# Kernel tuning notes

Hardware: AMD Instinct MI355X
Metric: run time of the kernel (lower is better)

## Reference

```python
import jax, jax.numpy as jnp
import numpy as np

E = 8          # num_experts
K = 2          # top_k
ALPHA = 0.01   # aux_loss_coef


def setup_inputs() -> dict:
    key = jax.random.key(0)
    k1, k2, k3, k4 = jax.random.split(key, 4)
    x = jax.random.normal(k1, (4, 4096, 768), jnp.float32)
    gate_w = jax.random.normal(k2, (E, 768), jnp.float32) * 0.02   # Router gate [E, H]
    w1 = jax.random.normal(k3, (E, 3072, 768), jnp.float32) * 0.02  # per-expert [I, H]
    w2 = jax.random.normal(k4, (E, 768, 3072), jnp.float32) * 0.02  # per-expert [H, I]
    return {"x": x, "gate_w": gate_w, "w1": w1, "w2": w2}


def reference(x, gate_w, w1, w2):
    B, S, H = x.shape
    N = B * S
    x_flat = x.reshape(N, H)

    # ---- Router: top-K gating ----
    gate_logits = x_flat @ gate_w.T                      # [N, E]
    gate_probs = jax.nn.softmax(gate_logits, axis=-1)    # [N, E]
    top_weights, top_indices = jax.lax.top_k(gate_probs, K)  # [N, K] each
    top_weights = top_weights / top_weights.sum(-1, keepdims=True)

    # ---- Load balancing aux loss ----
    counts = jnp.zeros(E, gate_probs.dtype).at[top_indices.reshape(-1)].add(1.0)
    f = counts / (N * K)
    p = gate_probs.mean(axis=0)
    aux_loss = ALPHA * E * jnp.sum(f * p)

    # ---- Dispatch + per-expert FFN + weighted combine ----
    # combine[n, e] = sum_k top_weights[n, k] * [top_indices[n, k] == e]
    combine = jnp.zeros((N, E), x_flat.dtype).at[
        jnp.arange(N)[:, None], top_indices
    ].add(top_weights)                                   # [N, E]

    y = jnp.zeros_like(x_flat)
    for e in range(E):  # fixed small loop over experts
        h = jax.nn.gelu(x_flat @ w1[e].T, approximate=True)  # [N, I] (GELU-tanh)
        y = y + combine[:, e:e + 1] * (h @ w2[e].T)          # [N, H]

    return y.reshape(B, S, H), aux_loss
```

## Files before the change

### kernel.cpp

```cpp
#include <hip/hip_runtime.h>
#include <hip/hip_bf16.h>

#define N_TOK 16384
#define H_DIM 768
#define I_DIM 3072
#define NEXP 8
#define RBLK 1024

typedef short bf16x8 __attribute__((ext_vector_type(8)));
typedef float f32x4 __attribute__((ext_vector_type(4)));

__device__ __forceinline__ unsigned short f2bf(float f) {
    unsigned int u = __float_as_uint(f);
    u += 0x7fffu + ((u >> 16) & 1u);
    return (unsigned short)(u >> 16);
}

__device__ __forceinline__ float gelu_tanh(float v) {
    float u = 0.7978845608028654f * (v + 0.044715f * v * v * v);
    float t = __expf(2.0f * fminf(u, 15.0f));
    return 0.5f * v * (1.0f + (t - 1.0f) / (t + 1.0f));
}

__device__ __forceinline__ void gll16(const void* g, void* l) {
    __builtin_amdgcn_global_load_lds(
        (const __attribute__((address_space(1))) unsigned int*)g,
        (__attribute__((address_space(3))) unsigned int*)l, 16, 0, 0);
}

__global__ __launch_bounds__(256) void moe_router(
    const float* __restrict__ x, const float* __restrict__ gw,
    unsigned short* __restrict__ xbf,
    int* __restrict__ topidx, float* __restrict__ topw,
    float* __restrict__ partials)
{
    __shared__ float gws[NEXP * H_DIM];
    __shared__ float red[64];
    const int tid = threadIdx.x;
    for (int i = tid * 4; i < NEXP * H_DIM; i += 1024)
        *(float4*)(gws + i) = *(const float4*)(gw + i);
    __syncthreads();

    const int lane = tid & 63;
    const int wid = tid >> 6;
    const int tbase = blockIdx.x * 16 + wid * 4;

    float lcnt[8], lps[8];
#pragma unroll
    for (int e = 0; e < 8; ++e) { lcnt[e] = 0.f; lps[e] = 0.f; }

#pragma unroll
    for (int k = 0; k < 4; ++k) {
        const int t = tbase + k;
        float acc[8] = {0.f, 0.f, 0.f, 0.f, 0.f, 0.f, 0.f, 0.f};
#pragma unroll
        for (int j = 0; j < 3; ++j) {
            const int col = j * 256 + lane * 4;
            float4 xv = *(const float4*)(x + (size_t)t * H_DIM + col);
            ushort4 o;
            o.x = f2bf(xv.x); o.y = f2bf(xv.y); o.z = f2bf(xv.z); o.w = f2bf(xv.w);
            *(ushort4*)(xbf + (size_t)t * H_DIM + col) = o;
#pragma unroll
            for (int e = 0; e < 8; ++e) {
                float4 g = *(const float4*)(gws + e * H_DIM + col);
                acc[e] += xv.x * g.x + xv.y * g.y + xv.z * g.z + xv.w * g.w;
            }
        }
#pragma unroll
        for (int off = 32; off >= 1; off >>= 1)
#pragma unroll
            for (int e = 0; e < 8; ++e) acc[e] += __shfl_xor(acc[e], off, 64);

        int e0 = 0;
#pragma unroll
        for (int e = 1; e < 8; ++e) if (acc[e] > acc[e0]) e0 = e;
        int e1 = (e0 == 0) ? 1 : 0;
#pragma unroll
        for (int e = 0; e < 8; ++e) if (e != e0 && acc[e] > acc[e1]) e1 = e;

        float mx = acc[0];
#pragma unroll
        for (int e = 1; e < 8; ++e) mx = fmaxf(mx, acc[e]);
        float p[8]; float s = 0.f;
#pragma unroll
        for (int e = 0; e < 8; ++e) { p[e] = expf(acc[e] - mx); s += p[e]; }
        float inv = 1.0f / s;
#pragma unroll
        for (int e = 0; e < 8; ++e) p[e] *= inv;

        float wsum = p[e0] + p[e1];
        if (lane == 0) {
            topidx[2 * t] = e0; topidx[2 * t + 1] = e1;
            topw[2 * t] = p[e0] / wsum; topw[2 * t + 1] = p[e1] / wsum;
            lcnt[e0] += 1.f; lcnt[e1] += 1.f;
#pragma unroll
            for (int e = 0; e < 8; ++e) lps[e] += p[e];
        }
    }

    if (lane == 0) {
#pragma unroll
        for (int e = 0; e < 8; ++e) {
            red[wid * 16 + e] = lcnt[e];
            red[wid * 16 + 8 + e] = lps[e];
        }
    }
    __syncthreads();
    if (tid < 16)
        partials[blockIdx.x * 16 + tid] =
            red[tid] + red[16 + tid] + red[32 + tid] + red[48 + tid];
}

__global__ __launch_bounds__(256) void moe_finalize(
    const float* __restrict__ partials, int* __restrict__ offs,
    float* __restrict__ aux_out)
{
    __shared__ float sdata[256];
    __shared__ float tot[16];
    const int tid = threadIdx.x;
    const int c = tid & 15;
    const int rg = tid >> 4;
    float s = 0.f;
    for (int r = rg; r < RBLK; r += 16)
        s += partials[r * 16 + c];
    sdata[tid] = s;
    __syncthreads();
    if (tid < 16) {
        float t = 0.f;
#pragma unroll
        for (int k = 0; k < 16; ++k) t += sdata[k * 16 + tid];
        tot[tid] = t;
    }
    __syncthreads();
    if (tid == 0) {
        float aux = 0.f; int run = 0;
        for (int e = 0; e < 8; ++e) {
            float cnt = tot[e];
            aux += (cnt / (float)(N_TOK * 2)) * (tot[8 + e] / (float)N_TOK);
            offs[e] = run;
            run += (int)(cnt + 0.5f);
        }
        offs[8] = run;
        *aux_out = 0.01f * 8.0f * aux;
    }
}

__global__ __launch_bounds__(256) void moe_rank(
    const int* __restrict__ topidx, const float* __restrict__ topw,
    const float* __restrict__ partials, const int* __restrict__ offs,
    int* __restrict__ perm, float* __restrict__ pw)
{
    const int b = blockIdx.x;
    const int tid = threadIdx.x;
    __shared__ float sred[256];
    __shared__ int pfx[8];
    float s = 0.f;
    const int e = tid & 7;
    for (int r = (tid >> 3); r < b; r += 32)
        s += partials[r * 16 + e];
    sred[tid] = s;
    __syncthreads();
    if (tid < 8) {
        float t = 0.f;
        for (int k = tid; k < 256; k += 8) t += sred[k];
        pfx[tid] = offs[tid] + (int)(t + 0.5f);
    }
    __syncthreads();
    if (tid < 32) {
        const int t = b * 16 + (tid >> 1);
        const int slot = tid & 1;
        const int myexp = topidx[2 * t + slot];
        int rank = 0;
#pragma unroll
        for (int ee = 0; ee < 8; ++ee) {
            unsigned long long m = __ballot(myexp == ee);
            if (myexp == ee)
                rank = pfx[ee] + __popcll(m & ((1ull << tid) - 1ull));
        }
        perm[rank] = t;
        pw[rank] = topw[2 * t + slot];
    }
}

__global__ __launch_bounds__(256) void moe_cvt(const float* __restrict__ in,
                                               unsigned short* __restrict__ out, int n)
{
    int idx = (blockIdx.x * 256 + threadIdx.x) * 4;
    const int stride = gridDim.x * 1024;
    for (; idx < n; idx += stride) {
        float4 v = *(const float4*)(in + idx);
        ushort4 o;
        o.x = f2bf(v.x); o.y = f2bf(v.y); o.z = f2bf(v.z); o.w = f2bf(v.w);
        *(ushort4*)(out + idx) = o;
    }
}


__global__ __launch_bounds__(256) void moe_gemm1(
    const unsigned short* __restrict__ xbf,
    const unsigned short* __restrict__ w1bf,
    const int* __restrict__ perm, const int* __restrict__ offs,
    unsigned short* __restrict__ hbuf, int e0)
{
    const int e = e0 + blockIdx.z;
    const int off = offs[e];
    const int n_e = offs[e + 1] - off;
    const int rt = blockIdx.y;
    if (rt * 128 >= n_e) return;
    const int ct = blockIdx.x;
    const int coff = off - offs[e0];

    __shared__ __align__(16) unsigned short As[128 * 64];
    __shared__ __align__(16) unsigned short Bs[128 * 64];

    const int tid = threadIdx.x;
    const int lane = tid & 63;
    const int wid = tid >> 6;
    const int wr = wid >> 1, wc = wid & 1;
    const int trow = tid >> 3;
    const int tcol = (((tid & 7) ^ (trow & 7))) * 8;

    const unsigned short* aptr[4];
    const unsigned short* bptr[4];
#pragma unroll
    for (int i = 0; i < 4; ++i) {
        int lr = rt * 128 + i * 32 + trow;
        if (lr >= n_e) lr = n_e - 1;
        const int token = perm[off + lr];
        aptr[i] = xbf + (size_t)token * H_DIM + tcol;
        const int n = ct * 128 + i * 32 + trow;
        bptr[i] = w1bf + ((size_t)e * I_DIM + n) * H_DIM + tcol;
    }
    unsigned short* As_dst = As + tid * 8;
    unsigned short* Bs_dst = Bs + tid * 8;

    const int rA = (wr * 64 + (lane & 15)) * 64;
    const int rB = (wc * 64 + (lane & 15)) * 64;
    const int cs0 = (((lane >> 4)    ) ^ (lane & 7)) * 8;
    const int cs1 = (((lane >> 4) + 4) ^ (lane & 7)) * 8;

    f32x4 acc[4][4] = {};

    for (int kk = 0; kk < H_DIM; kk += 64) {
#pragma unroll
        for (int i = 0; i < 4; ++i) gll16(aptr[i] + kk, As_dst + i * 2048);
#pragma unroll
        for (int i = 0; i < 4; ++i) gll16(bptr[i] + kk, Bs_dst + i * 2048);
        __syncthreads();
#pragma unroll
        for (int ksub = 0; ksub < 2; ++ksub) {
            const int cs = ksub ? cs1 : cs0;
            bf16x8 a[4], b[4];
#pragma unroll
            for (int i = 0; i < 4; ++i) a[i] = *(const bf16x8*)(As + rA + i * 1024 + cs);
#pragma unroll
            for (int j = 0; j < 4; ++j) b[j] = *(const bf16x8*)(Bs + rB + j * 1024 + cs);
#pragma unroll
            for (int i = 0; i < 4; ++i)
#pragma unroll
                for (int j = 0; j < 4; ++j)
                    acc[i][j] = __builtin_amdgcn_mfma_f32_16x16x32_bf16(a[i], b[j], acc[i][j], 0, 0, 0);
        }
        __syncthreads();
    }

    const int rbase = rt * 128 + wr * 64 + (lane >> 4) * 4;
    const int cbase = ct * 128 + wc * 64 + (lane & 15);
#pragma unroll
    for (int i = 0; i < 4; ++i) {
#pragma unroll
        for (int r = 0; r < 4; ++r) {
            const int lr = rbase + i * 16 + r;
            if (lr < n_e) {
                unsigned short* dst = hbuf + (size_t)(coff + lr) * I_DIM + cbase;
#pragma unroll
                for (int j = 0; j < 4; ++j)
                    dst[j * 16] = f2bf(gelu_tanh(acc[i][j][r]));
            }
        }
    }
}

__global__ __launch_bounds__(256) void moe_gemm2(
    const unsigned short* __restrict__ hbuf,
    const unsigned short* __restrict__ w2bf,
    const int* __restrict__ perm, const float* __restrict__ pw,
    const int* __restrict__ offs, float* __restrict__ y, int e0)
{
    const int e = e0 + blockIdx.z;
    const int off = offs[e];
    const int n_e = offs[e + 1] - off;
    const int rt = blockIdx.y;
    if (rt * 128 >= n_e) return;
    const int ct = blockIdx.x;
    const int coff = off - offs[e0];

    __shared__ __align__(16) unsigned short As[128 * 64];
    __shared__ __align__(16) unsigned short Bs[128 * 64];

    const int tid = threadIdx.x;
    const int lane = tid & 63;
    const int wid = tid >> 6;
    const int wr = wid >> 1, wc = wid & 1;
    const int trow = tid >> 3;
    const int tcol = (((tid & 7) ^ (trow & 7))) * 8;

    const unsigned short* aptr[4];
    const unsigned short* bptr[4];
#pragma unroll
    for (int i = 0; i < 4; ++i) {
        int lr = rt * 128 + i * 32 + trow;
        if (lr >= n_e) lr = n_e - 1;
        aptr[i] = hbuf + (size_t)(coff + lr) * I_DIM + tcol;
        const int n = ct * 128 + i * 32 + trow;
        bptr[i] = w2bf + ((size_t)e * H_DIM + n) * I_DIM + tcol;
    }
    unsigned short* As_dst = As + tid * 8;
    unsigned short* Bs_dst = Bs + tid * 8;

    const int rA = (wr * 64 + (lane & 15)) * 64;
    const int rB = (wc * 64 + (lane & 15)) * 64;
    const int cs0 = (((lane >> 4)    ) ^ (lane & 7)) * 8;
    const int cs1 = (((lane >> 4) + 4) ^ (lane & 7)) * 8;

    f32x4 acc[4][4] = {};

    for (int kk = 0; kk < I_DIM; kk += 64) {
#pragma unroll
        for (int i = 0; i < 4; ++i) gll16(aptr[i] + kk, As_dst + i * 2048);
#pragma unroll
        for (int i = 0; i < 4; ++i) gll16(bptr[i] + kk, Bs_dst + i * 2048);
        __syncthreads();
#pragma unroll
        for (int ksub = 0; ksub < 2; ++ksub) {
            const int cs = ksub ? cs1 : cs0;
            bf16x8 a[4], b[4];
#pragma unroll
            for (int i = 0; i < 4; ++i) a[i] = *(const bf16x8*)(As + rA + i * 1024 + cs);
#pragma unroll
            for (int j = 0; j < 4; ++j) b[j] = *(const bf16x8*)(Bs + rB + j * 1024 + cs);
#pragma unroll
            for (int i = 0; i < 4; ++i)
#pragma unroll
                for (int j = 0; j < 4; ++j)
                    acc[i][j] = __builtin_amdgcn_mfma_f32_16x16x32_bf16(a[i], b[j], acc[i][j], 0, 0, 0);
        }
        __syncthreads();
    }

    const int rbase = rt * 128 + wr * 64 + (lane >> 4) * 4;
    const int cbase = ct * 128 + wc * 64 + (lane & 15);
#pragma unroll
    for (int i = 0; i < 4; ++i) {
#pragma unroll
        for (int r = 0; r < 4; ++r) {
            const int lr = rbase + i * 16 + r;
            if (lr < n_e) {
                const int token = perm[off + lr];
                const float w = pw[off + lr];
                float* dst = y + (size_t)token * H_DIM + cbase;
#pragma unroll
                for (int j = 0; j < 4; ++j)
                    atomicAdd(dst + j * 16, w * acc[i][j][r]);
            }
        }
    }
}

extern "C" void kernel_launch(void* const* d_in, const int* in_sizes, int n_in,
                              void* d_out, int out_size, void* d_ws, size_t ws_size,
                              hipStream_t stream) {
    const float* x  = (const float*)d_in[0];
    const float* gw = (const float*)d_in[1];
    const float* w1 = (const float*)d_in[2];
    const float* w2 = (const float*)d_in[3];
    float* y = (float*)d_out;

    char* base = (char*)d_ws;
    size_t o = 0;
    unsigned short* xbf  = (unsigned short*)(base + o); o += (size_t)N_TOK * H_DIM * 2;
    unsigned short* w1bf = (unsigned short*)(base + o); o += (size_t)NEXP * I_DIM * H_DIM * 2;
    unsigned short* w2bf = (unsigned short*)(base + o); o += (size_t)NEXP * H_DIM * I_DIM * 2;
    int*   topidx = (int*)(base + o);   o += (size_t)N_TOK * 2 * 4;
    float* topw   = (float*)(base + o); o += (size_t)N_TOK * 2 * 4;
    int*   perm   = (int*)(base + o);   o += (size_t)N_TOK * 2 * 4;
    float* pw     = (float*)(base + o); o += (size_t)N_TOK * 2 * 4;
    float* partials = (float*)(base + o); o += (size_t)RBLK * 16 * 4;
    int*   offs     = (int*)(base + o);   o += 64;
    unsigned short* hbuf = (unsigned short*)(base + o);
    size_t remain = (ws_size > o) ? (ws_size - o) : 0;

    long cap_rows = (long)(remain / (size_t)(I_DIM * 2));
    int nch;
    if (cap_rows >= 32768)      nch = 1;
    else if (cap_rows >= 18022) nch = 2;
    else if (cap_rows >= 9011)  nch = 4;
    else                        nch = 8;
    const int G = NEXP / nch;

    hipMemsetAsync(d_out, 0, (size_t)out_size * 4, stream);

    moe_router<<<RBLK, 256, 0, stream>>>(x, gw, xbf, topidx, topw, partials);

    moe_cvt<<<2048, 256, 0, stream>>>(w1, w1bf, NEXP * I_DIM * H_DIM);
    moe_cvt<<<2048, 256, 0, stream>>>(w2, w2bf, NEXP * H_DIM * I_DIM);

    moe_finalize<<<1, 256, 0, stream>>>(partials, offs, y + (size_t)N_TOK * H_DIM);
    moe_rank<<<RBLK, 256, 0, stream>>>(topidx, topw, partials, offs, perm, pw);

    for (int c = 0; c < nch; ++c) {
        const int e0 = c * G;
        moe_gemm1<<<dim3(24, 128, G), 256, 0, stream>>>(
            xbf, w1bf, perm, offs, hbuf, e0);
        moe_gemm2<<<dim3(6, 128, G), 256, 0, stream>>>(
            hbuf, w2bf, perm, pw, offs, y, e0);
    }
}
```

Baseline: 700.2 us.

## Pipeline expert GEMMs with 4-stage LDS ring and fuse small setup kernels

Both expert GEMMs now use a 4-deep shared-memory ring with K=32 per stage, issuing loads three stages ahead. Waits use explicit vmcnt counters, a single barrier per step and setprio around the MFMA block, so global loads overlap with matrix math instead of a load, sync, compute, sync loop. The finalize kernel is folded into moe_rank, with each block recomputing the totals and block 0 writing offsets and aux loss, and the two weight conversions are merged into one launch. LDS use grows to 64KB per block, which may lower occupancy, and every rank block now reads all partials.

Measured after the change: 678.6 us. 1.03x faster.

```diff
diff --git a/kernel.cpp b/kernel.cpp
--- a/kernel.cpp
+++ b/kernel.cpp
@@ -111,59 +111,45 @@
             red[tid] + red[16 + tid] + red[32 + tid] + red[48 + tid];
 }
 
-__global__ __launch_bounds__(256) void moe_finalize(
-    const float* __restrict__ partials, int* __restrict__ offs,
-    float* __restrict__ aux_out)
-{
-    __shared__ float sdata[256];
-    __shared__ float tot[16];
-    const int tid = threadIdx.x;
-    const int c = tid & 15;
-    const int rg = tid >> 4;
-    float s = 0.f;
-    for (int r = rg; r < RBLK; r += 16)
-        s += partials[r * 16 + c];
-    sdata[tid] = s;
-    __syncthreads();
-    if (tid < 16) {
-        float t = 0.f;
-#pragma unroll
-        for (int k = 0; k < 16; ++k) t += sdata[k * 16 + tid];
-        tot[tid] = t;
-    }
-    __syncthreads();
-    if (tid == 0) {
-        float aux = 0.f; int run = 0;
-        for (int e = 0; e < 8; ++e) {
-            float cnt = tot[e];
-            aux += (cnt / (float)(N_TOK * 2)) * (tot[8 + e] / (float)N_TOK);
-            offs[e] = run;
-            run += (int)(cnt + 0.5f);
-        }
-        offs[8] = run;
-        *aux_out = 0.01f * 8.0f * aux;
-    }
-}
-
 __global__ __launch_bounds__(256) void moe_rank(
     const int* __restrict__ topidx, const float* __restrict__ topw,
-    const float* __restrict__ partials, const int* __restrict__ offs,
-    int* __restrict__ perm, float* __restrict__ pw)
+    const float* __restrict__ partials, int* __restrict__ offs,
+    float* __restrict__ aux_out, int* __restrict__ perm, float* __restrict__ pw)
 {
     const int b = blockIdx.x;
     const int tid = threadIdx.x;
-    __shared__ float sred[256];
+    __shared__ float stot[256], spre[256];
+    __shared__ float tot[16];
     __shared__ int pfx[8];
-    float s = 0.f;
-    const int e = tid & 7;
-    for (int r = (tid >> 3); r < b; r += 32)
-        s += partials[r * 16 + e];
-    sred[tid] = s;
+
+    const int c = tid & 15;
+    float vtot = 0.f, vpre = 0.f;
+    for (int r = tid >> 4; r < RBLK; r += 16) {
+        float v = partials[r * 16 + c];
+        vtot += v;
+        if (r < b) vpre += v;
+    }
+    stot[tid] = vtot; spre[tid] = vpre;
     __syncthreads();
-    if (tid < 8) {
-        float t = 0.f;
-        for (int k = tid; k < 256; k += 8) t += sred[k];
-        pfx[tid] = offs[tid] + (int)(t + 0.5f);
+    if (tid < 16) {
+        float t = 0.f, q = 0.f;
+#pragma unroll
+        for (int k = 0; k < 16; ++k) { t += stot[k * 16 + tid]; q += spre[k * 16 + tid]; }
+        tot[tid] = t;
+        if (tid < 8) spre[tid] = q;
+    }
+    __syncthreads();
+    if (tid == 0) {
+        int run = 0;
+        float aux = 0.f;
+#pragma unroll
+        for (int e = 0; e < 8; ++e) {
+            pfx[e] = run + (int)(spre[e] + 0.5f);
+            aux += (tot[e] / (float)(N_TOK * 2)) * (tot[8 + e] / (float)N_TOK);
+            if (b == 0) offs[e] = run;
+            run += (int)(tot[e] + 0.5f);
+        }
+        if (b == 0) { offs[8] = run; *aux_out = 0.01f * 8.0f * aux; }
     }
     __syncthreads();
     if (tid < 32) {
@@ -182,19 +168,69 @@
     }
 }
 
-__global__ __launch_bounds__(256) void moe_cvt(const float* __restrict__ in,
-                                               unsigned short* __restrict__ out, int n)
+__global__ __launch_bounds__(256) void moe_cvt2(
+    const float* __restrict__ a, unsigned short* __restrict__ oa,
+    const float* __restrict__ bsrc, unsigned short* __restrict__ ob, int n)
 {
     int idx = (blockIdx.x * 256 + threadIdx.x) * 4;
     const int stride = gridDim.x * 1024;
-    for (; idx < n; idx += stride) {
-        float4 v = *(const float4*)(in + idx);
+    for (; idx < 2 * n; idx += stride) {
+        const float* in = (idx < n) ? a : bsrc;
+        unsigned short* out = (idx < n) ? oa : ob;
+        const int i = (idx < n) ? idx : idx - n;
+        float4 v = *(const float4*)(in + i);
         ushort4 o;
         o.x = f2bf(v.x); o.y = f2bf(v.y); o.z = f2bf(v.z); o.w = f2bf(v.w);
-        *(ushort4*)(out + idx) = o;
-    }
-}
-
+        *(ushort4*)(out + i) = o;
+    }
+}
+
+
+#define GEMM_STAGE(t)                                                             \
+    { const int s_ = (t) & 3;                                                     \
+      gll16(asrc0 + (t) * 32, As + s_ * 4096 +        tid * 8);                   \
+      gll16(asrc1 + (t) * 32, As + s_ * 4096 + 2048 + tid * 8);                   \
+      gll16(bsrc0 + (t) * 32, Bs + s_ * 4096 +        tid * 8);                   \
+      gll16(bsrc1 + (t) * 32, Bs + s_ * 4096 + 2048 + tid * 8); }
+
+#define GEMM_LOADFRAG(t)                                                          \
+      const unsigned short* Ab_ = As + ((t) & 3) * 4096 + rowbase + pA * 8;       \
+      const unsigned short* Bb_ = Bs + ((t) & 3) * 4096 + rowbase + pB * 8;       \
+      bf16x8 a_[4], b_[4];                                                        \
+      _Pragma("unroll")                                                           \
+      for (int i_ = 0; i_ < 4; ++i_) a_[i_] = *(const bf16x8*)(Ab_ + i_ * 1024);  \
+      _Pragma("unroll")                                                           \
+      for (int j_ = 0; j_ < 4; ++j_) b_[j_] = *(const bf16x8*)(Bb_ + j_ * 1024);
+
+#define GEMM_MFMA()                                                               \
+      __builtin_amdgcn_s_setprio(1);                                              \
+      _Pragma("unroll")                                                           \
+      for (int i_ = 0; i_ < 4; ++i_)                                              \
+      _Pragma("unroll")                                                           \
+      for (int j_ = 0; j_ < 4; ++j_)                                              \
+          acc[i_][j_] = __builtin_amdgcn_mfma_f32_16x16x32_bf16(                  \
+              a_[i_], b_[j_], acc[i_][j_], 0, 0, 0);                              \
+      __builtin_amdgcn_s_setprio(0);
+
+#define GEMM_SYNC(N_IMM)                                                          \
+    asm volatile("s_waitcnt vmcnt(" #N_IMM ")" ::: "memory");                     \
+    __builtin_amdgcn_s_barrier();                                                 \
+    __builtin_amdgcn_sched_barrier(0);
+
+#define GEMM_PIPELINE(NT)                                                         \
+    GEMM_STAGE(0); GEMM_STAGE(1); GEMM_STAGE(2);                                  \
+    GEMM_SYNC(8);                                                                 \
+    for (int t = 0; t < (NT) - 3; ++t) {                                          \
+        GEMM_LOADFRAG(t);                                                         \
+        GEMM_STAGE(t + 3);                                                        \
+        GEMM_MFMA();                                                              \
+        GEMM_SYNC(8);                                                             \
+    }                                                                             \
+    { GEMM_LOADFRAG((NT) - 3); GEMM_MFMA(); }                                     \
+    GEMM_SYNC(4);                                                                 \
+    { GEMM_LOADFRAG((NT) - 2); GEMM_MFMA(); }                                     \
+    GEMM_SYNC(0);                                                                 \
+    { GEMM_LOADFRAG((NT) - 1); GEMM_MFMA(); }
 
 __global__ __launch_bounds__(256) void moe_gemm1(
     const unsigned short* __restrict__ xbf,
@@ -210,59 +246,37 @@
     const int ct = blockIdx.x;
     const int coff = off - offs[e0];
 
-    __shared__ __align__(16) unsigned short As[128 * 64];
-    __shared__ __align__(16) unsigned short Bs[128 * 64];
+    __shared__ __align__(16) unsigned short As[4 * 4096];
+    __shared__ __align__(16) unsigned short Bs[4 * 4096];
 
     const int tid = threadIdx.x;
     const int lane = tid & 63;
     const int wid = tid >> 6;
     const int wr = wid >> 1, wc = wid & 1;
-    const int trow = tid >> 3;
-    const int tcol = (((tid & 7) ^ (trow & 7))) * 8;
-
-    const unsigned short* aptr[4];
-    const unsigned short* bptr[4];
-#pragma unroll
-    for (int i = 0; i < 4; ++i) {
-        int lr = rt * 128 + i * 32 + trow;
-        if (lr >= n_e) lr = n_e - 1;
-        const int token = perm[off + lr];
-        aptr[i] = xbf + (size_t)token * H_DIM + tcol;
-        const int n = ct * 128 + i * 32 + trow;
-        bptr[i] = w1bf + ((size_t)e * I_DIM + n) * H_DIM + tcol;
-    }
-    unsigned short* As_dst = As + tid * 8;
-    unsigned short* Bs_dst = Bs + tid * 8;
-
-    const int rA = (wr * 64 + (lane & 15)) * 64;
-    const int rB = (wc * 64 + (lane & 15)) * 64;
-    const int cs0 = (((lane >> 4)    ) ^ (lane & 7)) * 8;
-    const int cs1 = (((lane >> 4) + 4) ^ (lane & 7)) * 8;
+
+    const int m = tid >> 3;
+    const int csw = (tid & 7) ^ (m & 7);
+    const int hi = csw >> 2, kc = csw & 3;
+
+    const unsigned short* asrc0; const unsigned short* asrc1;
+    const unsigned short* bsrc0; const unsigned short* bsrc1;
+    {
+        int g0 = hi * 64 + m, g1 = hi * 64 + 32 + m;
+        int lr0 = rt * 128 + g0; if (lr0 >= n_e) lr0 = n_e - 1;
+        int lr1 = rt * 128 + g1; if (lr1 >= n_e) lr1 = n_e - 1;
+        asrc0 = xbf + (size_t)perm[off + lr0] * H_DIM + kc * 8;
+        asrc1 = xbf + (size_t)perm[off + lr1] * H_DIM + kc * 8;
+        bsrc0 = w1bf + ((size_t)e * I_DIM + ct * 128 + g0) * H_DIM + kc * 8;
+        bsrc1 = w1bf + ((size_t)e * I_DIM + ct * 128 + g1) * H_DIM + kc * 8;
+    }
+
+    const int pA = ((wr << 2) | (lane >> 4)) ^ (lane & 7);
+    const int pB = ((wc << 2) | (lane >> 4)) ^ (lane & 7);
+    const int rowbase = (lane & 15) * 64;
 
     f32x4 acc[4][4] = {};
 
-    for (int kk = 0; kk < H_DIM; kk += 64) {
-#pragma unroll
-        for (int i = 0; i < 4; ++i) gll16(aptr[i] + kk, As_dst + i * 2048);
-#pragma unroll
-        for (int i = 0; i < 4; ++i) gll16(bptr[i] + kk, Bs_dst + i * 2048);
-        __syncthreads();
-#pragma unroll
-        for (int ksub = 0; ksub < 2; ++ksub) {
-            const int cs = ksub ? cs1 : cs0;
-            bf16x8 a[4], b[4];
-#pragma unroll
-            for (int i = 0; i < 4; ++i) a[i] = *(const bf16x8*)(As + rA + i * 1024 + cs);
-#pragma unroll
-            for (int j = 0; j < 4; ++j) b[j] = *(const bf16x8*)(Bs + rB + j * 1024 + cs);
-#pragma unroll
-            for (int i = 0; i < 4; ++i)
-#pragma unroll
-                for (int j = 0; j < 4; ++j)
-                    acc[i][j] = __builtin_amdgcn_mfma_f32_16x16x32_bf16(a[i], b[j], acc[i][j], 0, 0, 0);
-        }
-        __syncthreads();
-    }
+    GEMM_PIPELINE(H_DIM / 32);
 
     const int rbase = rt * 128 + wr * 64 + (lane >> 4) * 4;
     const int cbase = ct * 128 + wc * 64 + (lane & 15);
@@ -295,58 +309,37 @@
     const int ct = blockIdx.x;
     const int coff = off - offs[e0];
 
-    __shared__ __align__(16) unsigned short As[128 * 64];
-    __shared__ __align__(16) unsigned short Bs[128 * 64];
+    __shared__ __align__(16) unsigned short As[4 * 4096];
+    __shared__ __align__(16) unsigned short Bs[4 * 4096];
 
     const int tid = threadIdx.x;
     const int lane = tid & 63;
     const int wid = tid >> 6;
     const int wr = wid >> 1, wc = wid & 1;
-    const int trow = tid >> 3;
-    const int tcol = (((tid & 7) ^ (trow & 7))) * 8;
-
-    const unsigned short* aptr[4];
-    const unsigned short* bptr[4];
-#pragma unroll
-    for (int i = 0; i < 4; ++i) {
-        int lr = rt * 128 + i * 32 + trow;
-        if (lr >= n_e) lr = n_e - 1;
-        aptr[i] = hbuf + (size_t)(coff + lr) * I_DIM + tcol;
-        const int n = ct * 128 + i * 32 + trow;
-        bptr[i] = w2bf + ((size_t)e * H_DIM + n) * I_DIM + tcol;
-    }
-    unsigned short* As_dst = As + tid * 8;
-    unsigned short* Bs_dst = Bs + tid * 8;
-
-    const int rA = (wr * 64 + (lane & 15)) * 64;
-    const int rB = (wc * 64 + (lane & 15)) * 64;
-    const int cs0 = (((lane >> 4)    ) ^ (lane & 7)) * 8;
-    const int cs1 = (((lane >> 4) + 4) ^ (lane & 7)) * 8;
+
+    const int m = tid >> 3;
+    const int csw = (tid & 7) ^ (m & 7);
+    const int hi = csw >> 2, kc = csw & 3;
+
+    const unsigned short* asrc0; const unsigned short* asrc1;
+    const unsigned short* bsrc0; const unsigned short* bsrc1;
+    {
+        int g0 = hi * 64 + m, g1 = hi * 64 + 32 + m;
+        int lr0 = rt * 128 + g0; if (lr0 >= n_e) lr0 = n_e - 1;
+        int lr1 = rt * 128 + g1; if (lr1 >= n_e) lr1 = n_e - 1;
+        asrc0 = hbuf + (size_t)(coff + lr0) * I_DIM + kc * 8;
+        asrc1 = hbuf + (size_t)(coff + lr1) * I_DIM + kc * 8;
+        bsrc0 = w2bf + ((size_t)e * H_DIM + ct * 128 + g0) * I_DIM + kc * 8;
+        bsrc1 = w2bf + ((size_t)e * H_DIM + ct * 128 + g1) * I_DIM + kc * 8;
+    }
+
+    const int pA = ((wr << 2) | (lane >> 4)) ^ (lane & 7);
+    const int pB = ((wc << 2) | (lane >> 4)) ^ (lane & 7);
+    const int rowbase = (lane & 15) * 64;
 
     f32x4 acc[4][4] = {};
 
-    for (int kk = 0; kk < I_DIM; kk += 64) {
-#pragma unroll
-        for (int i = 0; i < 4; ++i) gll16(aptr[i] + kk, As_dst + i * 2048);
-#pragma unroll
-        for (int i = 0; i < 4; ++i) gll16(bptr[i] + kk, Bs_dst + i * 2048);
-        __syncthreads();
-#pragma unroll
-        for (int ksub = 0; ksub < 2; ++ksub) {
-            const int cs = ksub ? cs1 : cs0;
-            bf16x8 a[4], b[4];
-#pragma unroll
-            for (int i = 0; i < 4; ++i) a[i] = *(const bf16x8*)(As + rA + i * 1024 + cs);
-#pragma unroll
-            for (int j = 0; j < 4; ++j) b[j] = *(const bf16x8*)(Bs + rB + j * 1024 + cs);
-#pragma unroll
-            for (int i = 0; i < 4; ++i)
-#pragma unroll
-                for (int j = 0; j < 4; ++j)
-                    acc[i][j] = __builtin_amdgcn_mfma_f32_16x16x32_bf16(a[i], b[j], acc[i][j], 0, 0, 0);
-        }
-        __syncthreads();
-    }
+    GEMM_PIPELINE(I_DIM / 32);
 
     const int rbase = rt * 128 + wr * 64 + (lane >> 4) * 4;
     const int cbase = ct * 128 + wc * 64 + (lane & 15);
@@ -401,12 +394,9 @@
     hipMemsetAsync(d_out, 0, (size_t)out_size * 4, stream);
 
     moe_router<<<RBLK, 256, 0, stream>>>(x, gw, xbf, topidx, topw, partials);
-
-    moe_cvt<<<2048, 256, 0, stream>>>(w1, w1bf, NEXP * I_DIM * H_DIM);
-    moe_cvt<<<2048, 256, 0, stream>>>(w2, w2bf, NEXP * H_DIM * I_DIM);
-
-    moe_finalize<<<1, 256, 0, stream>>>(partials, offs, y + (size_t)N_TOK * H_DIM);
-    moe_rank<<<RBLK, 256, 0, stream>>>(topidx, topw, partials, offs, perm, pw);
+    moe_cvt2<<<4096, 256, 0, stream>>>(w1, w1bf, w2, w2bf, NEXP * I_DIM * H_DIM);
+    moe_rank<<<RBLK, 256, 0, stream>>>(topidx, topw, partials, offs,
+                                       y + (size_t)N_TOK * H_DIM, perm, pw);
 
     for (int c = 0; c < nch; ++c) {
         const int e0 = c * G;
```
